# Optimization experiments

Measured on AMD Instinct MI355X. Metric: run time of the kernel, lower is better.

## Reference

```python
import jax, jax.numpy as jnp
import numpy as np

HEADS = 16
DIM_HEAD = 64
QUERY_DIM = 1024


def setup_inputs() -> dict:
    key = jax.random.key(0)
    ks = jax.random.split(key, 5)
    B, S, D = 4, 2048, QUERY_DIM
    inner = HEADS * DIM_HEAD
    s = 0.02
    return {
        "x": jax.random.normal(ks[0], (B, S, D), dtype=jnp.float32),
        "Wq": jax.random.normal(ks[1], (D, inner), dtype=jnp.float32) * s,
        "Wk": jax.random.normal(ks[2], (D, inner), dtype=jnp.float32) * s,
        "Wv": jax.random.normal(ks[3], (D, inner), dtype=jnp.float32) * s,
        "Wo": jax.random.normal(ks[4], (inner, D), dtype=jnp.float32) * s,
    }


def reference(x, Wq, Wk, Wv, Wo):
    B, S, D = x.shape
    h, d = HEADS, DIM_HEAD
    scale = d ** (-0.5)
    # projections -> [B, h, S, d]
    q = (x @ Wq).reshape(B, S, h, d).transpose(0, 2, 1, 3)
    k = (x @ Wk).reshape(B, S, h, d).transpose(0, 2, 1, 3)
    v = (x @ Wv).reshape(B, S, h, d).transpose(0, 2, 1, 3)
    # scores [B, h, S, S]
    attn = jnp.einsum("bhqd,bhkd->bhqk", q, k) * scale
    attn = jax.nn.softmax(attn, axis=-1)
    out = jnp.einsum("bhqk,bhkd->bhqd", attn, v)
    out = out.transpose(0, 2, 1, 3).reshape(B, S, h * d)
    return out @ Wo
```

## Files before the change

kernel.cpp:

```cpp
#include <hip/hip_runtime.h>
#include <cstddef>

#define BATCH  4
#define SLEN   2048
#define NHEADS 16
#define DHEAD  64
#define DMODEL 1024

typedef __attribute__((ext_vector_type(8))) short short8;
typedef __attribute__((ext_vector_type(4))) float f32x4;

__device__ inline unsigned short f2bf(float f) {
    union { float f; unsigned int u; } v; v.f = f;
    unsigned int r = v.u + 0x7fffu + ((v.u >> 16) & 1u);
    return (unsigned short)(r >> 16);
}

__device__ inline float fast_exp2(float x) {
#if __has_builtin(__builtin_amdgcn_exp2f)
    return __builtin_amdgcn_exp2f(x);
#else
    return __expf(x * 0.69314718f);
#endif
}

__device__ inline void gload_lds16(const unsigned short* g, unsigned short* l) {
    __builtin_amdgcn_global_load_lds(
        (const __attribute__((address_space(1))) void*)g,
        (__attribute__((address_space(3))) void*)l, 16, 0, 0);
}

__global__ __launch_bounds__(256)
void convert_bf16(const float* __restrict__ src, unsigned short* __restrict__ dst, int n8)
{
    const int i = blockIdx.x * 256 + threadIdx.x;
    if (i >= n8) return;
    const float4 a = ((const float4*)src)[2 * i];
    const float4 b = ((const float4*)src)[2 * i + 1];
    short8 o;
    o[0] = (short)f2bf(a.x); o[1] = (short)f2bf(a.y);
    o[2] = (short)f2bf(a.z); o[3] = (short)f2bf(a.w);
    o[4] = (short)f2bf(b.x); o[5] = (short)f2bf(b.y);
    o[6] = (short)f2bf(b.z); o[7] = (short)f2bf(b.w);
    ((short8*)dst)[i] = o;
}

__global__ __launch_bounds__(256)
void wtrans(const float* __restrict__ W0, const float* __restrict__ W1,
            const float* __restrict__ W2, const float* __restrict__ W3,
            unsigned short* __restrict__ T0, unsigned short* __restrict__ T1,
            unsigned short* __restrict__ T2, unsigned short* __restrict__ T3)
{
    const int z = blockIdx.z;
    const float* W = (z == 0) ? W0 : (z == 1) ? W1 : (z == 2) ? W2 : W3;
    unsigned short* Wt = (z == 0) ? T0 : (z == 1) ? T1 : (z == 2) ? T2 : T3;

    __shared__ unsigned short T[64 * 72];
    const int tid = threadIdx.x;
    const int n0 = blockIdx.x * 64, k0 = blockIdx.y * 64;

    #pragma unroll
    for (int it = 0; it < 2; it++) {
        const int t2 = it * 256 + tid;
        const int row = t2 >> 3, col8 = (t2 & 7) * 8;
        const float4 a = *(const float4*)(W + (size_t)(k0 + row) * DMODEL + n0 + col8);
        const float4 b = *(const float4*)(W + (size_t)(k0 + row) * DMODEL + n0 + col8 + 4);
        short8 o;
        o[0] = (short)f2bf(a.x); o[1] = (short)f2bf(a.y);
        o[2] = (short)f2bf(a.z); o[3] = (short)f2bf(a.w);
        o[4] = (short)f2bf(b.x); o[5] = (short)f2bf(b.y);
        o[6] = (short)f2bf(b.z); o[7] = (short)f2bf(b.w);
        *(short8*)&T[row * 72 + col8] = o;
    }
    __syncthreads();
    #pragma unroll
    for (int it = 0; it < 2; it++) {
        const int t2 = it * 256 + tid;
        const int nn = t2 >> 3, k8 = (t2 & 7) * 8;
        short8 v;
        #pragma unroll
        for (int j = 0; j < 8; j++) v[j] = (short)T[(k8 + j) * 72 + nn];
        *(short8*)(Wt + (size_t)(n0 + nn) * DMODEL + k0 + k8) = v;
    }
}

template<int KIND>
__global__ __launch_bounds__(256)
void gemm_bf16(const unsigned short* __restrict__ A,
               const unsigned short* __restrict__ B0,
               const unsigned short* __restrict__ B1,
               const unsigned short* __restrict__ B2,
               void* __restrict__ C0v, void* __restrict__ C1v, void* __restrict__ C2v)
{
    constexpr int N = DMODEL, K = DMODEL;
    __shared__ unsigned short As[128 * 64];
    __shared__ unsigned short Bs[128 * 64];

    const int z = blockIdx.z;
    const unsigned short* Bw = (z == 0) ? B0 : (z == 1) ? B1 : B2;
    void* Cv = (z == 0) ? C0v : (z == 1) ? C1v : C2v;

    const int tid  = threadIdx.x;
    const int lane = tid & 63;
    const int wave = tid >> 6;
    const int c  = lane & 15, qd = lane >> 4;
    const int wr = wave >> 1, wc = wave & 1;
    const int m0 = blockIdx.y * 128, n0 = blockIdx.x * 128;

    const unsigned short* ag[4];
    const unsigned short* bg[4];
    unsigned short* al[4];
    unsigned short* bl[4];
    #pragma unroll
    for (int j = 0; j < 4; j++) {
        const int cid = j * 256 + tid;
        const int row = cid >> 3;
        const int k8  = (cid & 7) ^ (row & 7);
        ag[j] = A  + (size_t)(m0 + row) * K + k8 * 8;
        bg[j] = Bw + (size_t)(n0 + row) * K + k8 * 8;
        al[j] = &As[cid * 8];
        bl[j] = &Bs[cid * 8];
    }

    f32x4 acc[4][4];
    #pragma unroll
    for (int mb = 0; mb < 4; mb++)
        #pragma unroll
        for (int nb = 0; nb < 4; nb++)
            #pragma unroll
            for (int r = 0; r < 4; r++) acc[mb][nb][r] = 0.f;

    for (int k0 = 0; k0 < K; k0 += 64) {
        __syncthreads();
        #pragma unroll
        for (int j = 0; j < 4; j++) {
            gload_lds16(ag[j], al[j]);
            gload_lds16(bg[j], bl[j]);
            ag[j] += 64; bg[j] += 64;
        }
        __syncthreads();

        #pragma unroll
        for (int ks = 0; ks < 2; ks++) {
            const int sw = (ks * 4 + qd) ^ (c & 7);
            short8 af[4], bf[4];
            #pragma unroll
            for (int mb = 0; mb < 4; mb++)
                af[mb] = *(const short8*)&As[((wr * 64 + mb * 16 + c) * 8 + sw) * 8];
            #pragma unroll
            for (int nb = 0; nb < 4; nb++)
                bf[nb] = *(const short8*)&Bs[((wc * 64 + nb * 16 + c) * 8 + sw) * 8];
            #pragma unroll
            for (int mb = 0; mb < 4; mb++)
                #pragma unroll
                for (int nb = 0; nb < 4; nb++)
                    acc[mb][nb] = __builtin_amdgcn_mfma_f32_16x16x32_bf16(
                        af[mb], bf[nb], acc[mb][nb], 0, 0, 0);
        }
    }

    const int mbase = m0 + wr * 64 + qd * 4;
    const int nbase = n0 + wc * 64 + c;
    if (KIND == 1) {
        float* C = (float*)Cv;
        #pragma unroll
        for (int mb = 0; mb < 4; mb++)
            #pragma unroll
            for (int nb = 0; nb < 4; nb++)
                #pragma unroll
                for (int r = 0; r < 4; r++)
                    C[(size_t)(mbase + mb * 16 + r) * N + nbase + nb * 16] = acc[mb][nb][r];
    } else if (z != 2) {
        unsigned short* C = (unsigned short*)Cv;
        #pragma unroll
        for (int mb = 0; mb < 4; mb++)
            #pragma unroll
            for (int nb = 0; nb < 4; nb++)
                #pragma unroll
                for (int r = 0; r < 4; r++)
                    C[(size_t)(mbase + mb * 16 + r) * N + nbase + nb * 16] = f2bf(acc[mb][nb][r]);
    } else {
        unsigned short* C = (unsigned short*)Cv;
        const int b = mbase >> 11;
        #pragma unroll
        for (int mb = 0; mb < 4; mb++) {
            const int s = (mbase + mb * 16) & 2047;
            #pragma unroll
            for (int nb = 0; nb < 4; nb++) {
                const int n = nbase + nb * 16;
                const int h = n >> 6, dd = n & 63;
                ushort4 val = make_ushort4(f2bf(acc[mb][nb][0]), f2bf(acc[mb][nb][1]),
                                           f2bf(acc[mb][nb][2]), f2bf(acc[mb][nb][3]));
                *(ushort4*)(C + ((size_t)((b * 16 + h) * 64 + dd)) * SLEN + s) = val;
            }
        }
    }
}

__global__ __launch_bounds__(256, 2)
void attn_mfma3(const unsigned short* __restrict__ qb,
                const unsigned short* __restrict__ kb,
                const unsigned short* __restrict__ vtb,
                unsigned short* __restrict__ O)
{
    __shared__ unsigned short lds[26624];
    unsigned short* Ks = lds;
    unsigned short* Vs = lds + 4096;

    const int tid = threadIdx.x;
    const int w   = tid >> 6, ln = tid & 63;
    const int c   = ln & 15, qd = ln >> 4;
    unsigned short* Pw = lds + 8192 + w * 4608;

    const int qt = blockIdx.x, bh = blockIdx.y;
    const int b = bh >> 4, h = bh & 15;
    const size_t bh_base = ((size_t)b * SLEN * NHEADS + h) * 64;
    constexpr int RS = NHEADS * 64;
    constexpr float SCL2 = 0.18033688f;

    const int srow = ln >> 3;
    const int sk8  = (ln & 7) ^ srow;
    const unsigned short* kg0 = kb + bh_base + (size_t)(w * 8 + srow) * RS + sk8 * 8;
    const unsigned short* kg1 = kg0 + (size_t)32 * RS;
    const unsigned short* vg0 = vtb + ((size_t)bh * 64 + w * 8 + srow) * SLEN + sk8 * 8;
    const unsigned short* vg1 = vg0 + (size_t)32 * SLEN;
    unsigned short* kl0 = &Ks[(w * 64 + ln) * 8];
    unsigned short* kl1 = kl0 + 2048;
    unsigned short* vl0 = &Vs[(w * 64 + ln) * 8];
    unsigned short* vl1 = vl0 + 2048;

    short8 qf[4][2];
    #pragma unroll
    for (int qh = 0; qh < 4; qh++)
        #pragma unroll
        for (int ks = 0; ks < 2; ks++)
            qf[qh][ks] = *(const short8*)(qb + bh_base +
                (size_t)(qt * 256 + w * 64 + qh * 16 + c) * RS + ks * 32 + qd * 8);

    f32x4 acc[4][4];
    #pragma unroll
    for (int mb = 0; mb < 4; mb++)
        #pragma unroll
        for (int qh = 0; qh < 4; qh++)
            #pragma unroll
            for (int r = 0; r < 4; r++) acc[mb][qh][r] = 0.f;
    float lsum[4] = {0.f, 0.f, 0.f, 0.f};
    const int X0 = qd ^ (c & 7);
    const int X1 = (4 + qd) ^ (c & 7);

    for (int kt = 0; kt < SLEN / 64; kt++) {
        __syncthreads();
        gload_lds16(kg0, kl0); gload_lds16(kg1, kl1);
        gload_lds16(vg0, vl0); gload_lds16(vg1, vl1);
        kg0 += (size_t)64 * RS; kg1 += (size_t)64 * RS; vg0 += 64; vg1 += 64;
        __syncthreads();

        #pragma unroll
        for (int kbI = 0; kbI < 4; kbI++) {
            f32x4 sacc[4];
            #pragma unroll
            for (int qh = 0; qh < 4; qh++)
                #pragma unroll
                for (int r = 0; r < 4; r++) sacc[qh][r] = 0.f;
            #pragma unroll
            for (int ks = 0; ks < 2; ks++) {
                const int X = ks ? X1 : X0;
                short8 kf = *(const short8*)&Ks[((kbI * 16 + c) * 8 + X) * 8];
                #pragma unroll
                for (int qh = 0; qh < 4; qh++)
                    sacc[qh] = __builtin_amdgcn_mfma_f32_16x16x32_bf16(
                        kf, qf[qh][ks], sacc[qh], 0, 0, 0);
            }
            const int pchunk = ((kbI * 2 + (qd >> 1)) ^ (c & 7)) * 8 + (qd & 1) * 4;
            #pragma unroll
            for (int qh = 0; qh < 4; qh++) {
                const float p0 = fast_exp2(sacc[qh][0] * SCL2);
                const float p1 = fast_exp2(sacc[qh][1] * SCL2);
                const float p2 = fast_exp2(sacc[qh][2] * SCL2);
                const float p3 = fast_exp2(sacc[qh][3] * SCL2);
                lsum[qh] += (p0 + p1) + (p2 + p3);
                uint2 pk;
                pk.x = __builtin_amdgcn_perm(__float_as_uint(p1), __float_as_uint(p0), 0x07060302u);
                pk.y = __builtin_amdgcn_perm(__float_as_uint(p3), __float_as_uint(p2), 0x07060302u);
                *(uint2*)&Pw[(qh * 16 + c) * 64 + pchunk] = pk;
            }
        }
        __builtin_amdgcn_wave_barrier();

        #pragma unroll
        for (int ks = 0; ks < 2; ks++) {
            const int X = ks ? X1 : X0;
            short8 pf[4];
            #pragma unroll
            for (int qh = 0; qh < 4; qh++)
                pf[qh] = *(const short8*)&Pw[(qh * 16 + c) * 64 + X * 8];
            #pragma unroll
            for (int mb = 0; mb < 4; mb++) {
                short8 vf = *(const short8*)&Vs[((mb * 16 + c) * 8 + X) * 8];
                #pragma unroll
                for (int qh = 0; qh < 4; qh++)
                    acc[mb][qh] = __builtin_amdgcn_mfma_f32_16x16x32_bf16(
                        vf, pf[qh], acc[mb][qh], 0, 0, 0);
            }
        }
    }

    float inv[4];
    #pragma unroll
    for (int qh = 0; qh < 4; qh++) {
        float l = lsum[qh];
        l += __shfl_xor(l, 16);
        l += __shfl_xor(l, 32);
        inv[qh] = 1.001953125f / l;
    }
    __builtin_amdgcn_wave_barrier();
    #pragma unroll
    for (int mb = 0; mb < 4; mb++)
        #pragma unroll
        for (int qh = 0; qh < 4; qh++)
            #pragma unroll
            for (int r = 0; r < 4; r++)
                Pw[(qh * 16 + c) * 72 + mb * 16 + qd * 4 + r] =
                    f2bf(acc[mb][qh][r] * inv[qh]);
    __builtin_amdgcn_wave_barrier();
    #pragma unroll
    for (int it = 0; it < 8; it++) {
        const int t2 = it * 64 + ln;
        const int row = t2 >> 3, col8 = (t2 & 7) * 8;
        short8 o = *(const short8*)&Pw[row * 72 + col8];
        *(short8*)(O + bh_base + (size_t)(qt * 256 + w * 64 + row) * RS + col8) = o;
    }
}

extern "C" void kernel_launch(void* const* d_in, const int* in_sizes, int n_in,
                              void* d_out, int out_size, void* d_ws, size_t ws_size,
                              hipStream_t stream)
{
    const float* x  = (const float*)d_in[0];
    const float* Wq = (const float*)d_in[1];
    const float* Wk = (const float*)d_in[2];
    const float* Wv = (const float*)d_in[3];
    const float* Wo = (const float*)d_in[4];
    float* out = (float*)d_out;

    const size_t per = (size_t)BATCH * SLEN * NHEADS * DHEAD;
    const size_t wsz = (size_t)DMODEL * DMODEL;
    unsigned short* qb  = (unsigned short*)d_ws;
    unsigned short* kb  = qb  + per;
    unsigned short* vtb = kb  + per;
    unsigned short* xb  = vtb + per;
    unsigned short* wtq = xb  + per;
    unsigned short* wtk = wtq + wsz;
    unsigned short* wtv = wtk + wsz;
    unsigned short* wto = wtv + wsz;

    dim3 blk(256);
    convert_bf16<<<dim3((int)(per / 2048)), blk, 0, stream>>>(x, xb, (int)(per / 8));
    wtrans<<<dim3(16, 16, 4), blk, 0, stream>>>(Wq, Wk, Wv, Wo, wtq, wtk, wtv, wto);

    gemm_bf16<0><<<dim3(8, 64, 3), blk, 0, stream>>>(xb, wtq, wtk, wtv, qb, kb, vtb);

    attn_mfma3<<<dim3(SLEN / 256, BATCH * NHEADS), blk, 0, stream>>>(qb, kb, vtb, qb);

    gemm_bf16<1><<<dim3(8, 64, 1), blk, 0, stream>>>(qb, wto, wto, wto, out, out, out);
}
```

Measured before the change: 280.7 us.

## Use 32x32x16 MFMA in attention and keep P in registers instead of LDS

The attention kernel moves from 16x16x32 to 32x32x16 bf16 MFMA tiles. K rows are loaded into LDS in a permuted order so that the S accumulator layout lines up with the B-operand layout of the PV MFMA. The softmax probabilities can then be packed straight into registers as the PV operand, with no per-wave P round trip through LDS. This cuts LDS traffic and footprint, which may allow more occupancy, but it depends on the row permutation being correct and raises accumulator register pressure.

```diff
diff --git a/kernel.cpp b/kernel.cpp
--- a/kernel.cpp
+++ b/kernel.cpp
@@ -7,8 +7,9 @@
 #define DHEAD  64
 #define DMODEL 1024
 
-typedef __attribute__((ext_vector_type(8))) short short8;
-typedef __attribute__((ext_vector_type(4))) float f32x4;
+typedef __attribute__((ext_vector_type(8)))  short short8;
+typedef __attribute__((ext_vector_type(4)))  float f32x4;
+typedef __attribute__((ext_vector_type(16))) float f32x16;
 
 __device__ inline unsigned short f2bf(float f) {
     union { float f; unsigned int u; } v; v.f = f;
@@ -198,19 +199,19 @@
 }
 
 __global__ __launch_bounds__(256, 2)
-void attn_mfma3(const unsigned short* __restrict__ qb,
+void attn_mfma5(const unsigned short* __restrict__ qb,
                 const unsigned short* __restrict__ kb,
                 const unsigned short* __restrict__ vtb,
                 unsigned short* __restrict__ O)
 {
-    __shared__ unsigned short lds[26624];
+    __shared__ unsigned short lds[18432];
     unsigned short* Ks = lds;
     unsigned short* Vs = lds + 4096;
 
     const int tid = threadIdx.x;
     const int w   = tid >> 6, ln = tid & 63;
-    const int c   = ln & 15, qd = ln >> 4;
-    unsigned short* Pw = lds + 8192 + w * 4608;
+    const int c5  = ln & 31;
+    const int l5i = ln >> 5;
 
     const int qt = blockIdx.x, bh = blockIdx.y;
     const int b = bh >> 4, h = bh & 15;
@@ -220,7 +221,8 @@
 
     const int srow = ln >> 3;
     const int sk8  = (ln & 7) ^ srow;
-    const unsigned short* kg0 = kb + bh_base + (size_t)(w * 8 + srow) * RS + sk8 * 8;
+    const int prow = (srow & 3) | ((w & 1) << 2) | (((srow >> 2) & 1) << 3) | ((w >> 1) << 4);
+    const unsigned short* kg0 = kb + bh_base + (size_t)prow * RS + sk8 * 8;
     const unsigned short* kg1 = kg0 + (size_t)32 * RS;
     const unsigned short* vg0 = vtb + ((size_t)bh * 64 + w * 8 + srow) * SLEN + sk8 * 8;
     const unsigned short* vg1 = vg0 + (size_t)32 * SLEN;
@@ -229,24 +231,25 @@
     unsigned short* vl0 = &Vs[(w * 64 + ln) * 8];
     unsigned short* vl1 = vl0 + 2048;
 
-    short8 qf[4][2];
-    #pragma unroll
-    for (int qh = 0; qh < 4; qh++)
-        #pragma unroll
-        for (int ks = 0; ks < 2; ks++)
-            qf[qh][ks] = *(const short8*)(qb + bh_base +
-                (size_t)(qt * 256 + w * 64 + qh * 16 + c) * RS + ks * 32 + qd * 8);
-
-    f32x4 acc[4][4];
-    #pragma unroll
-    for (int mb = 0; mb < 4; mb++)
-        #pragma unroll
-        for (int qh = 0; qh < 4; qh++)
-            #pragma unroll
-            for (int r = 0; r < 4; r++) acc[mb][qh][r] = 0.f;
-    float lsum[4] = {0.f, 0.f, 0.f, 0.f};
-    const int X0 = qd ^ (c & 7);
-    const int X1 = (4 + qd) ^ (c & 7);
+    const int qtile = qt * 256 + w * 64;
+
+    short8 qf[2][4];
+    #pragma unroll
+    for (int qb2 = 0; qb2 < 2; qb2++)
+        #pragma unroll
+        for (int kst = 0; kst < 4; kst++)
+            qf[qb2][kst] = *(const short8*)(qb + bh_base +
+                (size_t)(qtile + qb2 * 32 + c5) * RS + kst * 16 + l5i * 8);
+
+    f32x16 acc[2][2];
+    #pragma unroll
+    for (int db = 0; db < 2; db++)
+        #pragma unroll
+        for (int qb2 = 0; qb2 < 2; qb2++)
+            #pragma unroll
+            for (int r = 0; r < 16; r++) acc[db][qb2][r] = 0.f;
+    float lsum[2] = {0.f, 0.f};
+    const int cl7 = c5 & 7;
 
     for (int kt = 0; kt < SLEN / 64; kt++) {
         __syncthreads();
@@ -256,79 +259,98 @@
         __syncthreads();
 
         #pragma unroll
-        for (int kbI = 0; kbI < 4; kbI++) {
-            f32x4 sacc[4];
-            #pragma unroll
-            for (int qh = 0; qh < 4; qh++)
-                #pragma unroll
-                for (int r = 0; r < 4; r++) sacc[qh][r] = 0.f;
-            #pragma unroll
-            for (int ks = 0; ks < 2; ks++) {
-                const int X = ks ? X1 : X0;
-                short8 kf = *(const short8*)&Ks[((kbI * 16 + c) * 8 + X) * 8];
-                #pragma unroll
-                for (int qh = 0; qh < 4; qh++)
-                    sacc[qh] = __builtin_amdgcn_mfma_f32_16x16x32_bf16(
-                        kf, qf[qh][ks], sacc[qh], 0, 0, 0);
-            }
-            const int pchunk = ((kbI * 2 + (qd >> 1)) ^ (c & 7)) * 8 + (qd & 1) * 4;
-            #pragma unroll
-            for (int qh = 0; qh < 4; qh++) {
-                const float p0 = fast_exp2(sacc[qh][0] * SCL2);
-                const float p1 = fast_exp2(sacc[qh][1] * SCL2);
-                const float p2 = fast_exp2(sacc[qh][2] * SCL2);
-                const float p3 = fast_exp2(sacc[qh][3] * SCL2);
-                lsum[qh] += (p0 + p1) + (p2 + p3);
-                uint2 pk;
-                pk.x = __builtin_amdgcn_perm(__float_as_uint(p1), __float_as_uint(p0), 0x07060302u);
-                pk.y = __builtin_amdgcn_perm(__float_as_uint(p3), __float_as_uint(p2), 0x07060302u);
-                *(uint2*)&Pw[(qh * 16 + c) * 64 + pchunk] = pk;
+        for (int kb32 = 0; kb32 < 2; kb32++) {
+            f32x16 sacc[2];
+            #pragma unroll
+            for (int qb2 = 0; qb2 < 2; qb2++)
+                #pragma unroll
+                for (int r = 0; r < 16; r++) sacc[qb2][r] = 0.f;
+            #pragma unroll
+            for (int kst = 0; kst < 4; kst++) {
+                const int slot = (kst * 2 + l5i) ^ cl7;
+                short8 kf = *(const short8*)&Ks[((kb32 * 32 + c5) * 8 + slot) * 8];
+                #pragma unroll
+                for (int qb2 = 0; qb2 < 2; qb2++)
+                    sacc[qb2] = __builtin_amdgcn_mfma_f32_32x32x16_bf16(
+                        kf, qf[qb2][kst], sacc[qb2], 0, 0, 0);
+            }
+
+            unsigned pk[2][8];
+            #pragma unroll
+            for (int qb2 = 0; qb2 < 2; qb2++) {
+                float p[16];
+                float s0 = 0.f, s1 = 0.f;
+                #pragma unroll
+                for (int r = 0; r < 16; r += 2) {
+                    p[r]     = fast_exp2(sacc[qb2][r]     * SCL2);
+                    p[r + 1] = fast_exp2(sacc[qb2][r + 1] * SCL2);
+                    s0 += p[r]; s1 += p[r + 1];
+                }
+                lsum[qb2] += s0 + s1;
+                #pragma unroll
+                for (int i = 0; i < 8; i++)
+                    pk[qb2][i] = __builtin_amdgcn_perm(
+                        __float_as_uint(p[2 * i + 1]), __float_as_uint(p[2 * i]),
+                        0x07060302u);
+            }
+
+            #pragma unroll
+            for (int kk = 0; kk < 2; kk++) {
+                const int k2 = kb32 * 2 + kk;
+                short8 pf[2];
+                #pragma unroll
+                for (int qb2 = 0; qb2 < 2; qb2++) {
+                    union { unsigned u[4]; short8 s; } t;
+                    t.u[0] = pk[qb2][4 * kk + 0];
+                    t.u[1] = pk[qb2][4 * kk + 1];
+                    t.u[2] = pk[qb2][4 * kk + 2];
+                    t.u[3] = pk[qb2][4 * kk + 3];
+                    pf[qb2] = t.s;
+                }
+                #pragma unroll
+                for (int db = 0; db < 2; db++) {
+                    const int slot = (k2 * 2 + l5i) ^ cl7;
+                    short8 vf = *(const short8*)&Vs[((db * 32 + c5) * 8 + slot) * 8];
+                    #pragma unroll
+                    for (int qb2 = 0; qb2 < 2; qb2++)
+                        acc[db][qb2] = __builtin_amdgcn_mfma_f32_32x32x16_bf16(
+                            vf, pf[qb2], acc[db][qb2], 0, 0, 0);
+                }
             }
         }
-        __builtin_amdgcn_wave_barrier();
-
-        #pragma unroll
-        for (int ks = 0; ks < 2; ks++) {
-            const int X = ks ? X1 : X0;
-            short8 pf[4];
-            #pragma unroll
-            for (int qh = 0; qh < 4; qh++)
-                pf[qh] = *(const short8*)&Pw[(qh * 16 + c) * 64 + X * 8];
-            #pragma unroll
-            for (int mb = 0; mb < 4; mb++) {
-                short8 vf = *(const short8*)&Vs[((mb * 16 + c) * 8 + X) * 8];
-                #pragma unroll
-                for (int qh = 0; qh < 4; qh++)
-                    acc[mb][qh] = __builtin_amdgcn_mfma_f32_16x16x32_bf16(
-                        vf, pf[qh], acc[mb][qh], 0, 0, 0);
-            }
-        }
-    }
-
-    float inv[4];
-    #pragma unroll
-    for (int qh = 0; qh < 4; qh++) {
-        float l = lsum[qh];
-        l += __shfl_xor(l, 16);
+    }
+
+    __syncthreads();
+    float inv[2];
+    #pragma unroll
+    for (int qb2 = 0; qb2 < 2; qb2++) {
+        float l = lsum[qb2];
         l += __shfl_xor(l, 32);
-        inv[qh] = 1.001953125f / l;
-    }
-    __builtin_amdgcn_wave_barrier();
-    #pragma unroll
-    for (int mb = 0; mb < 4; mb++)
-        #pragma unroll
-        for (int qh = 0; qh < 4; qh++)
-            #pragma unroll
-            for (int r = 0; r < 4; r++)
-                Pw[(qh * 16 + c) * 72 + mb * 16 + qd * 4 + r] =
-                    f2bf(acc[mb][qh][r] * inv[qh]);
+        inv[qb2] = 1.001953125f / l;
+    }
+    unsigned short* E = lds + w * 4608;
+    #pragma unroll
+    for (int db = 0; db < 2; db++)
+        #pragma unroll
+        for (int qb2 = 0; qb2 < 2; qb2++)
+            #pragma unroll
+            for (int u = 0; u < 4; u++) {
+                const int d0 = db * 32 + 8 * u + 4 * l5i;
+                const int q  = qb2 * 32 + c5;
+                ushort4 val = make_ushort4(
+                    f2bf(acc[db][qb2][4 * u + 0] * inv[qb2]),
+                    f2bf(acc[db][qb2][4 * u + 1] * inv[qb2]),
+                    f2bf(acc[db][qb2][4 * u + 2] * inv[qb2]),
+                    f2bf(acc[db][qb2][4 * u + 3] * inv[qb2]));
+                *(ushort4*)&E[q * 72 + d0] = val;
+            }
     __builtin_amdgcn_wave_barrier();
     #pragma unroll
     for (int it = 0; it < 8; it++) {
         const int t2 = it * 64 + ln;
         const int row = t2 >> 3, col8 = (t2 & 7) * 8;
-        short8 o = *(const short8*)&Pw[row * 72 + col8];
-        *(short8*)(O + bh_base + (size_t)(qt * 256 + w * 64 + row) * RS + col8) = o;
+        short8 o = *(const short8*)&E[row * 72 + col8];
+        *(short8*)(O + bh_base + (size_t)(qtile + row) * RS + col8) = o;
     }
 }
 
@@ -360,7 +382,7 @@
 
     gemm_bf16<0><<<dim3(8, 64, 3), blk, 0, stream>>>(xb, wtq, wtk, wtv, qb, kb, vtb);
 
-    attn_mfma3<<<dim3(SLEN / 256, BATCH * NHEADS), blk, 0, stream>>>(qb, kb, vtb, qb);
+    attn_mfma5<<<dim3(SLEN / 256, BATCH * NHEADS), blk, 0, stream>>>(qb, kb, vtb, qb);
 
     gemm_bf16<1><<<dim3(8, 64, 1), blk, 0, stream>>>(qb, wto, wto, wto, out, out, out);
 }
```

Result: faster. 274.1 us (-2.4%).
